# Performance work log

Measured on AMD Instinct MI355X. Metric: run time of the kernel, lower is better.

Reference implementation:

```python
import jax, jax.numpy as jnp
import numpy as np

N_NODES = 100000
N_EDGES = 3200000
IN_CH = 128
HID = 8
HEADS = 8
NEG_SLOPE = 0.2  # PyG GATConv default


def setup_inputs() -> dict:
    key = jax.random.key(0)
    ks = jax.random.split(key, 12)
    s = 0.1
    return {
        "x": jax.random.normal(ks[0], (N_NODES, IN_CH), jnp.float32),
        "edge_index": jax.random.randint(ks[1], (2, N_EDGES), 0, N_NODES, dtype=jnp.int64),
        "W1": jax.random.normal(ks[2], (IN_CH, HEADS * HID), jnp.float32) * s,
        "a_src1": jax.random.normal(ks[3], (1, HEADS, HID), jnp.float32) * s,
        "a_dst1": jax.random.normal(ks[4], (1, HEADS, HID), jnp.float32) * s,
        "b1": jax.random.normal(ks[5], (HEADS * HID,), jnp.float32) * s,
        "W2": jax.random.normal(ks[6], (HEADS * HID, HID), jnp.float32) * s,
        "a_src2": jax.random.normal(ks[7], (1, 1, HID), jnp.float32) * s,
        "a_dst2": jax.random.normal(ks[8], (1, 1, HID), jnp.float32) * s,
        "b2": jax.random.normal(ks[9], (HID,), jnp.float32) * s,
        "Wc": jax.random.normal(ks[10], (HID, 2), jnp.float32) * s,
        "bc": jax.random.normal(ks[11], (2,), jnp.float32) * s,
    }


def gat_conv(x, src, dst, W, a_src, a_dst, b, concat):
    """PyG-style GATConv (eval mode, self-loops already appended to src/dst)."""
    n = x.shape[0]
    H, C = a_src.shape[1], a_src.shape[2]
    h = (x @ W).reshape(n, H, C)                       # [N,H,C]
    alpha_src = jnp.sum(h * a_src, axis=-1)            # [N,H]
    alpha_dst = jnp.sum(h * a_dst, axis=-1)            # [N,H]
    e = jax.nn.leaky_relu(alpha_src[src] + alpha_dst[dst], NEG_SLOPE)  # [E,H]
    # segment softmax over destination-node neighborhoods
    m = jax.ops.segment_max(e, dst, num_segments=n)    # [N,H]
    m = jnp.where(jnp.isfinite(m), m, 0.0)
    p = jnp.exp(e - m[dst])
    z = jax.ops.segment_sum(p, dst, num_segments=n)    # [N,H]
    alpha = p / (z[dst] + 1e-16)                       # [E,H]
    out = jax.ops.segment_sum(alpha[..., None] * h[src], dst, num_segments=n)  # [N,H,C]
    out = out.reshape(n, H * C) if concat else out.mean(axis=1)
    return out + b


def reference(x, edge_index, W1, a_src1, a_dst1, b1, W2, a_src2, a_dst2, b2, Wc, bc):
    n = x.shape[0]
    loops = jnp.arange(n, dtype=edge_index.dtype)
    src = jnp.concatenate([edge_index[0], loops])
    dst = jnp.concatenate([edge_index[1], loops])
    h = jax.nn.relu(gat_conv(x, src, dst, W1, a_src1, a_dst1, b1, concat=True))
    embeddings = gat_conv(h, src, dst, W2, a_src2, a_dst2, b2, concat=False)
    logits = embeddings @ Wc + bc
    return embeddings, logits
```

## Files before the change

### kernel.cpp

```cpp
#include <hip/hip_runtime.h>
#include <hip/hip_bf16.h>
#include <hip/hip_fp16.h>

#define NN 100000
#define IN_CH 128
#define HID 8
#define HEADS 8
#define HC 64
#define BSH 8
#define NBUCK ((NN + 255) >> 8)
#define NBLK 512
#define PCAP 10240
#define LOG2E 1.44269504088896340736f

__device__ __forceinline__ unsigned short f2bf(float f) {
    unsigned u = __float_as_uint(f);
    unsigned r = (u + 0x7fffu + ((u >> 16) & 1u)) >> 16;
    return (unsigned short)r;
}


__global__ __launch_bounds__(256) void k_bincount(const int* __restrict__ ei, int E, int ET,
                                                  int cpb, int* __restrict__ cnt) {
    __shared__ int h[NBUCK];
    for (int i = threadIdx.x; i < NBUCK; i += 256) h[i] = 0;
    __syncthreads();
    int beg = blockIdx.x * cpb, end = min(ET, beg + cpb);
    for (int t = beg + threadIdx.x; t < end; t += 256) {
        int d = (t < E) ? ei[E + t] : (t - E);
        atomicAdd(&h[d >> BSH], 1);
    }
    __syncthreads();
    for (int i = threadIdx.x; i < NBUCK; i += 256) cnt[i * NBLK + blockIdx.x] = h[i];
}

__global__ __launch_bounds__(256) void k_colscan(int* __restrict__ cnt, int* __restrict__ btot) {
    __shared__ int sd[256];
    int t = threadIdx.x;
    int* col = cnt + blockIdx.x * NBLK;
    int v0 = col[2 * t], v1 = col[2 * t + 1];
    int s = v0 + v1;
    sd[t] = s;
    __syncthreads();
    for (int off = 1; off < 256; off <<= 1) {
        int u = (t >= off) ? sd[t - off] : 0;
        __syncthreads();
        sd[t] += u;
        __syncthreads();
    }
    int excl = sd[t] - s;
    col[2 * t] = excl;
    col[2 * t + 1] = excl + v0;
    if (t == 255) btot[blockIdx.x] = excl + s;
}

__global__ __launch_bounds__(256) void k_bucketbase(const int* __restrict__ btot,
                                                    int* __restrict__ bbase,
                                                    int* __restrict__ row_ptr) {
    __shared__ int sd[256];
    int t = threadIdx.x;
    int v0 = (2 * t < NBUCK) ? btot[2 * t] : 0;
    int v1 = (2 * t + 1 < NBUCK) ? btot[2 * t + 1] : 0;
    int s = v0 + v1;
    sd[t] = s;
    __syncthreads();
    for (int off = 1; off < 256; off <<= 1) {
        int u = (t >= off) ? sd[t - off] : 0;
        __syncthreads();
        sd[t] += u;
        __syncthreads();
    }
    int excl = sd[t] - s;
    if (2 * t < NBUCK) bbase[2 * t] = excl;
    if (2 * t + 1 < NBUCK) bbase[2 * t + 1] = excl + v0;
    if (t == 255) { bbase[NBUCK] = excl + s; row_ptr[NN] = excl + s; }
}

__global__ __launch_bounds__(256) void k_binscatter(const int* __restrict__ ei, int E, int ET,
                                                    int cpb, const int* __restrict__ cnt,
                                                    const int* __restrict__ bbase,
                                                    unsigned* __restrict__ pairs) {
    __shared__ int cur[NBUCK];
    for (int i = threadIdx.x; i < NBUCK; i += 256)
        cur[i] = bbase[i] + cnt[i * NBLK + blockIdx.x];
    __syncthreads();
    int beg = blockIdx.x * cpb, end = min(ET, beg + cpb);
    for (int t = beg + threadIdx.x; t < end; t += 256) {
        int s, d;
        if (t < E) { s = ei[t]; d = ei[E + t]; } else { s = t - E; d = t - E; }
        int pos = atomicAdd(&cur[d >> BSH], 1);
        pairs[pos] = ((unsigned)s << 8) | (unsigned)(d & 255);
    }
}

__global__ __launch_bounds__(256) void k_bucketscatter(const unsigned* __restrict__ pairs,
                                                       const int* __restrict__ bbase,
                                                       int* __restrict__ row_ptr,
                                                       int* __restrict__ csr) {
    __shared__ unsigned pl[PCAP];
    __shared__ int h[256];
    __shared__ int sd[256];
    int b = blockIdx.x;
    int t = threadIdx.x;
    int beg = bbase[b], end = bbase[b + 1];
    int cntE = end - beg;
    bool inl = cntE <= PCAP;
    if (inl)
        for (int j = t; j < cntE; j += 256) pl[j] = pairs[beg + j];
    h[t] = 0;
    __syncthreads();
    for (int j = t; j < cntE; j += 256) {
        unsigned pv = inl ? pl[j] : pairs[beg + j];
        atomicAdd(&h[pv & 255u], 1);
    }
    __syncthreads();
    int v = h[t];
    sd[t] = v;
    __syncthreads();
    for (int off = 1; off < 256; off <<= 1) {
        int u = (t >= off) ? sd[t - off] : 0;
        __syncthreads();
        sd[t] += u;
        __syncthreads();
    }
    int excl = sd[t] - v;
    int node = (b << 8) + t;
    if (node < NN) row_ptr[node] = beg + excl;
    __syncthreads();
    h[t] = beg + excl;
    __syncthreads();
    for (int j = t; j < cntE; j += 256) {
        unsigned pv = inl ? pl[j] : pairs[beg + j];
        int pos = atomicAdd(&h[pv & 255u], 1);
        csr[pos] = (int)(pv >> 8);
    }
}


__global__ __launch_bounds__(256) void k_gemm1(const float* __restrict__ x,
                                               const float* __restrict__ W1,
                                               const float* __restrict__ aS,
                                               const float* __restrict__ aD,
                                               unsigned* __restrict__ h1q,
                                               unsigned* __restrict__ asc1,
                                               float* __restrict__ adst1) {
    __shared__ float wl[IN_CH * HC];
    int tid = threadIdx.x;
    {
        const float4* Wg4 = (const float4*)W1;
        float4* wl4 = (float4*)wl;
#pragma unroll
        for (int i = 0; i < 8; ++i) wl4[tid + i * 256] = Wg4[tid + i * 256];
    }
    __syncthreads();
    int lane = tid & 63;
    int row = blockIdx.x * 16 + (tid >> 6) * 4 + (lane >> 4);
    int c0 = (lane & 15) * 4;
    const float4* xr = (const float4*)(x + (size_t)row * IN_CH);
    float4 acc = make_float4(0.f, 0.f, 0.f, 0.f);
#pragma unroll 4
    for (int kq = 0; kq < IN_CH / 4; ++kq) {
        float4 xv = xr[kq];
        const float4* wrow = (const float4*)(wl + (kq * 4) * HC + c0);
        float4 w0 = wrow[0];
        float4 w1 = wrow[HC / 4];
        float4 w2 = wrow[2 * (HC / 4)];
        float4 w3 = wrow[3 * (HC / 4)];
        acc.x += xv.x * w0.x + xv.y * w1.x + xv.z * w2.x + xv.w * w3.x;
        acc.y += xv.x * w0.y + xv.y * w1.y + xv.z * w2.y + xv.w * w3.y;
        acc.z += xv.x * w0.z + xv.y * w1.z + xv.z * w2.z + xv.w * w3.z;
        acc.w += xv.x * w0.w + xv.y * w1.w + xv.z * w2.w + xv.w * w3.w;
    }
    float am = fmaxf(fmaxf(fabsf(acc.x), fabsf(acc.y)), fmaxf(fabsf(acc.z), fabsf(acc.w)));
    am = fmaxf(am, __shfl_xor(am, 1, 64));
    am = fmaxf(am, __shfl_xor(am, 2, 64));
    am = fmaxf(am, __shfl_xor(am, 4, 64));
    am = fmaxf(am, __shfl_xor(am, 8, 64));
    am = fmaxf(am, 1e-20f);
    float qinv = 127.0f / am;
    int q0 = __float2int_rn(acc.x * qinv) + 128;
    int q1 = __float2int_rn(acc.y * qinv) + 128;
    int q2 = __float2int_rn(acc.z * qinv) + 128;
    int q3 = __float2int_rn(acc.w * qinv) + 128;
    unsigned u = (unsigned)q0 | ((unsigned)q1 << 8) | ((unsigned)q2 << 16) | ((unsigned)q3 << 24);
    h1q[row * 16 + (lane & 15)] = u;
    int head = (lane & 15) >> 1;
    int cl = c0 & 7;
    const float* as = aS + head * 8 + cl;
    const float* ad = aD + head * 8 + cl;
    float ps = acc.x * as[0] + acc.y * as[1] + acc.z * as[2] + acc.w * as[3];
    float pd = acc.x * ad[0] + acc.y * ad[1] + acc.z * ad[2] + acc.w * ad[3];
    ps += __shfl_xor(ps, 1, 64);
    pd += __shfl_xor(pd, 1, 64);
    if ((lane & 1) == 0) {
        unsigned lo = (unsigned)__half_as_ushort(__float2half(ps * LOG2E));
        unsigned hi = (unsigned)__half_as_ushort(__float2half(am * (1.0f / 127.0f)));
        asc1[row * 8 + head] = lo | (hi << 16);
        adst1[row * 8 + head] = pd * LOG2E;
    }
}


__global__ __launch_bounds__(256) void k_agg1(const int* __restrict__ row_ptr,
                                              const int* __restrict__ csr,
                                              const unsigned* __restrict__ asc1,
                                              const float* __restrict__ adst1,
                                              const uint2* __restrict__ h1q,
                                              const float* __restrict__ b1,
                                              const float* __restrict__ W2,
                                              const float* __restrict__ aS2,
                                              const float* __restrict__ aD2,
                                              unsigned short* __restrict__ h2bf,
                                              float* __restrict__ asrc2,
                                              float* __restrict__ adst2) {
    int tid = threadIdx.x;
    int lane = tid & 63;
    int slot = lane >> 3;
    int hl = lane & 7;
    float w2r[8];
#pragma unroll
    for (int i = 0; i < 8; ++i) w2r[i] = W2[(hl * 8 + i) * 8 + slot];
    float4 b0 = *(const float4*)(b1 + hl * 8);
    float4 b1v = *(const float4*)(b1 + hl * 8 + 4);
    float as2 = aS2[slot], ad2 = aD2[slot];
    int nbase = (blockIdx.x * 4 + (tid >> 6)) * 4;
    for (int ni = 0; ni < 4; ++ni) {
        int n = nbase + ni;
        float adst = adst1[n * 8 + hl];
        int beg = row_ptr[n], end = row_ptr[n + 1];
        int nit = (end - beg + 7) >> 3;
        float z = 0.f, zs = 0.f;
        float4 accA = make_float4(0.f, 0.f, 0.f, 0.f);
        float4 accB = make_float4(0.f, 0.f, 0.f, 0.f);
        int j0 = beg + slot;
        bool v0 = j0 < end;
        int s0 = v0 ? csr[j0] : 0;
        int j1 = j0 + 8;
        bool v1 = j1 < end;
        int s1 = v1 ? csr[j1] : 0;
        unsigned a0 = asc1[(size_t)s0 * 8 + hl];
        uint2 r0 = h1q[(size_t)s0 * 8 + hl];
        int jn = j1;
        for (int it = 0; it < nit; ++it) {
            int j2 = jn + 8;
            bool v2 = j2 < end;
            int s2 = v2 ? csr[j2] : 0;
            unsigned a1 = asc1[(size_t)s1 * 8 + hl];
            uint2 r1 = h1q[(size_t)s1 * 8 + hl];
            float e = __half2float(__ushort_as_half((unsigned short)(a0 & 0xffffu))) + adst;
            float csc = __half2float(__ushort_as_half((unsigned short)(a0 >> 16)));
            e = fmaxf(e, 0.2f * e);
            float p = v0 ? exp2f(e) : 0.f;
            float ps = p * csc;
            z += p;
            zs += ps;
            accA.x += ps * (float)(r0.x & 255u);
            accA.y += ps * (float)((r0.x >> 8) & 255u);
            accA.z += ps * (float)((r0.x >> 16) & 255u);
            accA.w += ps * (float)(r0.x >> 24);
            accB.x += ps * (float)(r0.y & 255u);
            accB.y += ps * (float)((r0.y >> 8) & 255u);
            accB.z += ps * (float)((r0.y >> 16) & 255u);
            accB.w += ps * (float)(r0.y >> 24);
            v0 = v1; a0 = a1; r0 = r1;
            v1 = v2; s1 = s2;
            jn = j2;
        }
#pragma unroll
        for (int off = 8; off <= 32; off <<= 1) {
            z += __shfl_xor(z, off, 64);
            zs += __shfl_xor(zs, off, 64);
            accA.x += __shfl_xor(accA.x, off, 64);
            accA.y += __shfl_xor(accA.y, off, 64);
            accA.z += __shfl_xor(accA.z, off, 64);
            accA.w += __shfl_xor(accA.w, off, 64);
            accB.x += __shfl_xor(accB.x, off, 64);
            accB.y += __shfl_xor(accB.y, off, 64);
            accB.z += __shfl_xor(accB.z, off, 64);
            accB.w += __shfl_xor(accB.w, off, 64);
        }
        float inv = 1.f / (z + 1e-16f);
        float zc = 128.f * zs;
        float hr0 = fmaxf((accA.x - zc) * inv + b0.x, 0.f);
        float hr1 = fmaxf((accA.y - zc) * inv + b0.y, 0.f);
        float hr2 = fmaxf((accA.z - zc) * inv + b0.z, 0.f);
        float hr3 = fmaxf((accA.w - zc) * inv + b0.w, 0.f);
        float hr4 = fmaxf((accB.x - zc) * inv + b1v.x, 0.f);
        float hr5 = fmaxf((accB.y - zc) * inv + b1v.y, 0.f);
        float hr6 = fmaxf((accB.z - zc) * inv + b1v.z, 0.f);
        float hr7 = fmaxf((accB.w - zc) * inv + b1v.w, 0.f);
        float part = hr0 * w2r[0] + hr1 * w2r[1] + hr2 * w2r[2] + hr3 * w2r[3] +
                     hr4 * w2r[4] + hr5 * w2r[5] + hr6 * w2r[6] + hr7 * w2r[7];
        part += __shfl_xor(part, 1, 64);
        part += __shfl_xor(part, 2, 64);
        part += __shfl_xor(part, 4, 64);
        if (hl == 0) {
            h2bf[(size_t)n * 8 + slot] = f2bf(part);
            float s2v = part * as2;
            float d2v = part * ad2;
            s2v += __shfl_xor(s2v, 8, 64);
            s2v += __shfl_xor(s2v, 16, 64);
            s2v += __shfl_xor(s2v, 32, 64);
            d2v += __shfl_xor(d2v, 8, 64);
            d2v += __shfl_xor(d2v, 16, 64);
            d2v += __shfl_xor(d2v, 32, 64);
            if (slot == 0) {
                asrc2[n] = s2v * LOG2E;
                adst2[n] = d2v * LOG2E;
            }
        }
    }
}


__global__ __launch_bounds__(256) void k_agg2(const int* __restrict__ row_ptr,
                                              const int* __restrict__ csr,
                                              const float* __restrict__ asrc2,
                                              const float* __restrict__ adst2,
                                              const unsigned short* __restrict__ h2bf,
                                              const float* __restrict__ b2,
                                              const float* __restrict__ Wc,
                                              const float* __restrict__ bc,
                                              float* __restrict__ out) {
    int tid = threadIdx.x;
    int lane = tid & 63;
    int n = blockIdx.x * 4 + (tid >> 6);
    int slot = lane >> 3;
    int sl = lane & 7;
    float adst = adst2[n];
    int beg = row_ptr[n], end = row_ptr[n + 1];
    int nit = (end - beg + 7) >> 3;
    float z = 0.f, acc = 0.f;
    int j0 = beg + slot;
    bool v0 = j0 < end;
    int s0 = v0 ? csr[j0] : 0;
    int j1 = j0 + 8;
    bool v1 = j1 < end;
    int s1 = v1 ? csr[j1] : 0;
    float a0 = asrc2[s0];
    unsigned short u0 = h2bf[(size_t)s0 * 8 + sl];
    int jn = j1;
    for (int it = 0; it < nit; ++it) {
        int j2 = jn + 8;
        bool v2 = j2 < end;
        int s2 = v2 ? csr[j2] : 0;
        float a1 = asrc2[s1];
        unsigned short u1 = h2bf[(size_t)s1 * 8 + sl];
        float e = a0 + adst;
        e = fmaxf(e, 0.2f * e);
        float p = v0 ? exp2f(e) : 0.f;
        float h0 = __uint_as_float(((unsigned)u0) << 16);
        z += p;
        acc += p * h0;
        v0 = v1; a0 = a1; u0 = u1;
        v1 = v2; s1 = s2;
        jn = j2;
    }
#pragma unroll
    for (int off = 8; off <= 32; off <<= 1) {
        z += __shfl_xor(z, off, 64);
        acc += __shfl_xor(acc, off, 64);
    }
    float emb = acc / (z + 1e-16f) + b2[sl];
    if (slot == 0) out[(size_t)n * HID + sl] = emb;
    float t0 = emb * Wc[sl * 2 + 0];
    float t1 = emb * Wc[sl * 2 + 1];
    t0 += __shfl_xor(t0, 1, 64); t0 += __shfl_xor(t0, 2, 64); t0 += __shfl_xor(t0, 4, 64);
    t1 += __shfl_xor(t1, 1, 64); t1 += __shfl_xor(t1, 2, 64); t1 += __shfl_xor(t1, 4, 64);
    if (lane == 0) {
        out[(size_t)NN * HID + n * 2 + 0] = t0 + bc[0];
        out[(size_t)NN * HID + n * 2 + 1] = t1 + bc[1];
    }
}


extern "C" void kernel_launch(void* const* d_in, const int* in_sizes, int n_in,
                              void* d_out, int out_size, void* d_ws, size_t ws_size,
                              hipStream_t stream) {
    const float* x  = (const float*)d_in[0];
    const int*   ei = (const int*)d_in[1];
    const float* W1 = (const float*)d_in[2];
    const float* aS = (const float*)d_in[3];
    const float* aD = (const float*)d_in[4];
    const float* b1 = (const float*)d_in[5];
    const float* W2 = (const float*)d_in[6];
    const float* aS2 = (const float*)d_in[7];
    const float* aD2 = (const float*)d_in[8];
    const float* b2 = (const float*)d_in[9];
    const float* Wc = (const float*)d_in[10];
    const float* bc = (const float*)d_in[11];

    int E = in_sizes[1] / 2;
    int N = NN;
    int ET = E + N;
    int cpb = (ET + NBLK - 1) / NBLK;

    char* p = (char*)d_ws;
    auto alloc = [&](size_t bytes) -> char* {
        char* r = p;
        p += (bytes + 255) & ~(size_t)255;
        return r;
    };
    unsigned* h1q   = (unsigned*)alloc((size_t)N * 16 * 4);
    unsigned* asc1  = (unsigned*)alloc((size_t)N * 8 * 4);
    float* adst1    = (float*)alloc((size_t)N * 8 * 4);
    unsigned short* h2bf = (unsigned short*)alloc((size_t)N * 8 * 2);
    float* asrc2    = (float*)alloc((size_t)N * 4);
    float* adst2    = (float*)alloc((size_t)N * 4);
    int*   row_ptr  = (int*)alloc((size_t)(N + 1) * 4);
    int*   cnt      = (int*)alloc((size_t)NBUCK * NBLK * 4);
    int*   btot     = (int*)alloc((size_t)NBUCK * 4);
    int*   bbase    = (int*)alloc((size_t)(NBUCK + 1) * 4);
    int*   csr      = (int*)alloc((size_t)ET * 4);
    unsigned* pairs = (unsigned*)alloc((size_t)ET * 4);

    k_bincount<<<NBLK, 256, 0, stream>>>(ei, E, ET, cpb, cnt);
    k_colscan<<<NBUCK, 256, 0, stream>>>(cnt, btot);
    k_bucketbase<<<1, 256, 0, stream>>>(btot, bbase, row_ptr);
    k_binscatter<<<NBLK, 256, 0, stream>>>(ei, E, ET, cpb, cnt, bbase, pairs);
    k_bucketscatter<<<NBUCK, 256, 0, stream>>>(pairs, bbase, row_ptr, csr);

    k_gemm1<<<N / 16, 256, 0, stream>>>(x, W1, aS, aD, h1q, asc1, adst1);
    k_agg1<<<N / 16, 256, 0, stream>>>(row_ptr, csr, asc1, adst1, (const uint2*)h1q,
                                       b1, W2, aS2, aD2, h2bf, asrc2, adst2);
    k_agg2<<<N / 4, 256, 0, stream>>>(row_ptr, csr, asrc2, adst2, h2bf, b2, Wc, bc,
                                      (float*)d_out);
}
```

Before: 240.4 us.

## Fuse CSR bucket scatter into layer-1 aggregation and split source score/scale arrays

Removes the separate bucket-scatter kernel and folds CSR construction into a new aggregation kernel. Each 256-node bucket is now handled by two blocks, one per 128-node half. Both blocks rebuild the bucket histogram and scan; each then scatters only its own half's edges into global CSR and, when they fit, into a shared-memory copy that its aggregation loop reads. The packed half-precision source score plus scale word becomes a separate fp16 array and a per-node float scale array. The goal is to drop a kernel launch and the global CSR re-read. In exchange there are far fewer, longer-running blocks with 32 nodes per wave processed serially, duplicated histogram work, and an extra per-edge gather for the scale.

```diff
diff --git a/kernel.cpp b/kernel.cpp
--- a/kernel.cpp
+++ b/kernel.cpp
@@ -10,7 +10,7 @@
 #define BSH 8
 #define NBUCK ((NN + 255) >> 8)
 #define NBLK 512
-#define PCAP 10240
+#define PCAP2 5120
 #define LOG2E 1.44269504088896340736f
 
 __device__ __forceinline__ unsigned short f2bf(float f) {
@@ -93,56 +93,14 @@
     }
 }
 
-__global__ __launch_bounds__(256) void k_bucketscatter(const unsigned* __restrict__ pairs,
-                                                       const int* __restrict__ bbase,
-                                                       int* __restrict__ row_ptr,
-                                                       int* __restrict__ csr) {
-    __shared__ unsigned pl[PCAP];
-    __shared__ int h[256];
-    __shared__ int sd[256];
-    int b = blockIdx.x;
-    int t = threadIdx.x;
-    int beg = bbase[b], end = bbase[b + 1];
-    int cntE = end - beg;
-    bool inl = cntE <= PCAP;
-    if (inl)
-        for (int j = t; j < cntE; j += 256) pl[j] = pairs[beg + j];
-    h[t] = 0;
-    __syncthreads();
-    for (int j = t; j < cntE; j += 256) {
-        unsigned pv = inl ? pl[j] : pairs[beg + j];
-        atomicAdd(&h[pv & 255u], 1);
-    }
-    __syncthreads();
-    int v = h[t];
-    sd[t] = v;
-    __syncthreads();
-    for (int off = 1; off < 256; off <<= 1) {
-        int u = (t >= off) ? sd[t - off] : 0;
-        __syncthreads();
-        sd[t] += u;
-        __syncthreads();
-    }
-    int excl = sd[t] - v;
-    int node = (b << 8) + t;
-    if (node < NN) row_ptr[node] = beg + excl;
-    __syncthreads();
-    h[t] = beg + excl;
-    __syncthreads();
-    for (int j = t; j < cntE; j += 256) {
-        unsigned pv = inl ? pl[j] : pairs[beg + j];
-        int pos = atomicAdd(&h[pv & 255u], 1);
-        csr[pos] = (int)(pv >> 8);
-    }
-}
-
 
 __global__ __launch_bounds__(256) void k_gemm1(const float* __restrict__ x,
                                                const float* __restrict__ W1,
                                                const float* __restrict__ aS,
                                                const float* __restrict__ aD,
                                                unsigned* __restrict__ h1q,
-                                               unsigned* __restrict__ asc1,
+                                               unsigned short* __restrict__ asrc1h,
+                                               float* __restrict__ scale1,
                                                float* __restrict__ adst1) {
     __shared__ float wl[IN_CH * HC];
     int tid = threadIdx.x;
@@ -193,28 +151,77 @@
     ps += __shfl_xor(ps, 1, 64);
     pd += __shfl_xor(pd, 1, 64);
     if ((lane & 1) == 0) {
-        unsigned lo = (unsigned)__half_as_ushort(__float2half(ps * LOG2E));
-        unsigned hi = (unsigned)__half_as_ushort(__float2half(am * (1.0f / 127.0f)));
-        asc1[row * 8 + head] = lo | (hi << 16);
+        asrc1h[row * 8 + head] = __half_as_ushort(__float2half(ps * LOG2E));
         adst1[row * 8 + head] = pd * LOG2E;
     }
-}
-
-
-__global__ __launch_bounds__(256) void k_agg1(const int* __restrict__ row_ptr,
-                                              const int* __restrict__ csr,
-                                              const unsigned* __restrict__ asc1,
-                                              const float* __restrict__ adst1,
-                                              const uint2* __restrict__ h1q,
-                                              const float* __restrict__ b1,
-                                              const float* __restrict__ W2,
-                                              const float* __restrict__ aS2,
-                                              const float* __restrict__ aD2,
-                                              unsigned short* __restrict__ h2bf,
-                                              float* __restrict__ asrc2,
-                                              float* __restrict__ adst2) {
-    int tid = threadIdx.x;
-    int lane = tid & 63;
+    if ((lane & 15) == 0) scale1[row] = am * (1.0f / 127.0f);
+}
+
+
+__global__ __launch_bounds__(256) void k_sortagg1(const unsigned* __restrict__ pairs,
+                                                  const int* __restrict__ bbase,
+                                                  int* __restrict__ row_ptr,
+                                                  int* __restrict__ csr,
+                                                  const unsigned short* __restrict__ asrc1h,
+                                                  const float* __restrict__ scale1,
+                                                  const float* __restrict__ adst1,
+                                                  const uint2* __restrict__ h1q,
+                                                  const float* __restrict__ b1,
+                                                  const float* __restrict__ W2,
+                                                  const float* __restrict__ aS2,
+                                                  const float* __restrict__ aD2,
+                                                  unsigned short* __restrict__ h2bf,
+                                                  float* __restrict__ asrc2,
+                                                  float* __restrict__ adst2) {
+    __shared__ int csr_l[PCAP2];
+    __shared__ int hist[256];
+    __shared__ int sdn[256];
+    __shared__ int rs[129];
+    int t = threadIdx.x;
+    int sb = blockIdx.x >> 1;
+    int hf = blockIdx.x & 1;
+    int beg = bbase[sb], end = bbase[sb + 1];
+    hist[t] = 0;
+    __syncthreads();
+    for (int j = beg + t; j < end; j += 256)
+        atomicAdd(&hist[pairs[j] & 255u], 1);
+    __syncthreads();
+    int v = hist[t];
+    sdn[t] = v;
+    __syncthreads();
+    for (int off = 1; off < 256; off <<= 1) {
+        int u = (t >= off) ? sdn[t - off] : 0;
+        __syncthreads();
+        sdn[t] += u;
+        __syncthreads();
+    }
+    int excl = sdn[t] - v;
+    int half0cnt = sdn[127];
+    int mybase = beg + (hf ? half0cnt : 0);
+    int myend = hf ? end : (beg + half0cnt);
+    bool inl = (myend - mybase) <= PCAP2;
+    bool own = (t >> 7) == hf;
+    if (own) {
+        int node = (sb << 8) + t;
+        if (node < NN) row_ptr[node] = beg + excl;
+        rs[t & 127] = beg + excl;
+        if ((t & 127) == 127) rs[128] = myend;
+    }
+    hist[t] = beg + excl;
+    __syncthreads();
+    for (int j = beg + t; j < end; j += 256) {
+        unsigned pv = pairs[j];
+        int d = (int)(pv & 255u);
+        if ((d >> 7) == hf) {
+            int pos = atomicAdd(&hist[d], 1);
+            int src = (int)(pv >> 8);
+            csr[pos] = src;
+            if (inl) csr_l[pos - mybase] = src;
+        }
+    }
+    __syncthreads();
+    int lane = t & 63;
+    int wv = t >> 6;
     int slot = lane >> 3;
     int hl = lane & 7;
     float w2r[8];
@@ -223,35 +230,34 @@
     float4 b0 = *(const float4*)(b1 + hl * 8);
     float4 b1v = *(const float4*)(b1 + hl * 8 + 4);
     float as2 = aS2[slot], ad2 = aD2[slot];
-    int nbase = (blockIdx.x * 4 + (tid >> 6)) * 4;
-    for (int ni = 0; ni < 4; ++ni) {
-        int n = nbase + ni;
-        float adst = adst1[n * 8 + hl];
-        int beg = row_ptr[n], end = row_ptr[n + 1];
-        int nit = (end - beg + 7) >> 3;
+    for (int i = 0; i < 32; ++i) {
+        int ln = wv * 32 + i;
+        int node = (sb << 8) + hf * 128 + ln;
+        if (node >= NN) break;
+        float adst = adst1[node * 8 + hl];
+        int jb = rs[ln] - mybase;
+        int je = rs[ln + 1] - mybase;
+        int nit = (je - jb + 7) >> 3;
         float z = 0.f, zs = 0.f;
         float4 accA = make_float4(0.f, 0.f, 0.f, 0.f);
         float4 accB = make_float4(0.f, 0.f, 0.f, 0.f);
-        int j0 = beg + slot;
-        bool v0 = j0 < end;
-        int s0 = v0 ? csr[j0] : 0;
-        int j1 = j0 + 8;
-        bool v1 = j1 < end;
-        int s1 = v1 ? csr[j1] : 0;
-        unsigned a0 = asc1[(size_t)s0 * 8 + hl];
+        int j = jb + slot;
+        bool v0 = j < je;
+        int s0 = v0 ? (inl ? csr_l[j] : csr[mybase + j]) : 0;
+        unsigned short a0 = asrc1h[(size_t)s0 * 8 + hl];
+        float c0s = scale1[s0];
         uint2 r0 = h1q[(size_t)s0 * 8 + hl];
-        int jn = j1;
         for (int it = 0; it < nit; ++it) {
-            int j2 = jn + 8;
-            bool v2 = j2 < end;
-            int s2 = v2 ? csr[j2] : 0;
-            unsigned a1 = asc1[(size_t)s1 * 8 + hl];
+            int j1 = j + 8;
+            bool v1 = j1 < je;
+            int s1 = v1 ? (inl ? csr_l[j1] : csr[mybase + j1]) : 0;
+            unsigned short a1 = asrc1h[(size_t)s1 * 8 + hl];
+            float c1s = scale1[s1];
             uint2 r1 = h1q[(size_t)s1 * 8 + hl];
-            float e = __half2float(__ushort_as_half((unsigned short)(a0 & 0xffffu))) + adst;
-            float csc = __half2float(__ushort_as_half((unsigned short)(a0 >> 16)));
+            float e = __half2float(__ushort_as_half(a0)) + adst;
             e = fmaxf(e, 0.2f * e);
             float p = v0 ? exp2f(e) : 0.f;
-            float ps = p * csc;
+            float ps = p * c0s;
             z += p;
             zs += ps;
             accA.x += ps * (float)(r0.x & 255u);
@@ -262,9 +268,8 @@
             accB.y += ps * (float)((r0.y >> 8) & 255u);
             accB.z += ps * (float)((r0.y >> 16) & 255u);
             accB.w += ps * (float)(r0.y >> 24);
-            v0 = v1; a0 = a1; r0 = r1;
-            v1 = v2; s1 = s2;
-            jn = j2;
+            v0 = v1; a0 = a1; c0s = c1s; r0 = r1;
+            j = j1;
         }
 #pragma unroll
         for (int off = 8; off <= 32; off <<= 1) {
@@ -295,7 +300,7 @@
         part += __shfl_xor(part, 2, 64);
         part += __shfl_xor(part, 4, 64);
         if (hl == 0) {
-            h2bf[(size_t)n * 8 + slot] = f2bf(part);
+            h2bf[(size_t)node * 8 + slot] = f2bf(part);
             float s2v = part * as2;
             float d2v = part * ad2;
             s2v += __shfl_xor(s2v, 8, 64);
@@ -305,8 +310,8 @@
             d2v += __shfl_xor(d2v, 16, 64);
             d2v += __shfl_xor(d2v, 32, 64);
             if (slot == 0) {
-                asrc2[n] = s2v * LOG2E;
-                adst2[n] = d2v * LOG2E;
+                asrc2[node] = s2v * LOG2E;
+                adst2[node] = d2v * LOG2E;
             }
         }
     }
@@ -402,7 +407,8 @@
         return r;
     };
     unsigned* h1q   = (unsigned*)alloc((size_t)N * 16 * 4);
-    unsigned* asc1  = (unsigned*)alloc((size_t)N * 8 * 4);
+    unsigned short* asrc1h = (unsigned short*)alloc((size_t)N * 8 * 2);
+    float* scale1   = (float*)alloc((size_t)N * 4);
     float* adst1    = (float*)alloc((size_t)N * 8 * 4);
     unsigned short* h2bf = (unsigned short*)alloc((size_t)N * 8 * 2);
     float* asrc2    = (float*)alloc((size_t)N * 4);
@@ -418,11 +424,11 @@
     k_colscan<<<NBUCK, 256, 0, stream>>>(cnt, btot);
     k_bucketbase<<<1, 256, 0, stream>>>(btot, bbase, row_ptr);
     k_binscatter<<<NBLK, 256, 0, stream>>>(ei, E, ET, cpb, cnt, bbase, pairs);
-    k_bucketscatter<<<NBUCK, 256, 0, stream>>>(pairs, bbase, row_ptr, csr);
-
-    k_gemm1<<<N / 16, 256, 0, stream>>>(x, W1, aS, aD, h1q, asc1, adst1);
-    k_agg1<<<N / 16, 256, 0, stream>>>(row_ptr, csr, asc1, adst1, (const uint2*)h1q,
-                                       b1, W2, aS2, aD2, h2bf, asrc2, adst2);
+
+    k_gemm1<<<N / 16, 256, 0, stream>>>(x, W1, aS, aD, h1q, asrc1h, scale1, adst1);
+    k_sortagg1<<<2 * NBUCK, 256, 0, stream>>>(pairs, bbase, row_ptr, csr,
+                                              asrc1h, scale1, adst1, (const uint2*)h1q,
+                                              b1, W2, aS2, aD2, h2bf, asrc2, adst2);
     k_agg2<<<N / 4, 256, 0, stream>>>(row_ptr, csr, asrc2, adst2, h2bf, b2, Wc, bc,
                                       (float*)d_out);
 }
```

Result: slower. 277.8 us (+15.6%).

## Register-block GEMM over four rows, split per-node scale, batch agg2 nodes

Applied to the files above, without the earlier changes.

k_gemm1 now computes four rows per thread, so each W1 value read from LDS is reused four times, and it launches 64 rows per block with a clamp for the tail. The per-head packed (alpha_src, scale) word is split into a half-precision alpha_src array plus one float scale per node, which shrinks the per-edge gather in k_agg1 but adds a second small scattered load per edge. k_agg2 processes four nodes per wavefront, cutting block count and hoisting the bias and classifier weight loads. The risks are higher register pressure in the GEMM and an extra memory transaction per edge in aggregation.

```diff
diff --git a/kernel.cpp b/kernel.cpp
--- a/kernel.cpp
+++ b/kernel.cpp
@@ -142,7 +142,8 @@
                                                const float* __restrict__ aS,
                                                const float* __restrict__ aD,
                                                unsigned* __restrict__ h1q,
-                                               unsigned* __restrict__ asc1,
+                                               unsigned short* __restrict__ asrc1h,
+                                               float* __restrict__ scale1,
                                                float* __restrict__ adst1) {
     __shared__ float wl[IN_CH * HC];
     int tid = threadIdx.x;
@@ -154,56 +155,86 @@
     }
     __syncthreads();
     int lane = tid & 63;
-    int row = blockIdx.x * 16 + (tid >> 6) * 4 + (lane >> 4);
+    int wv = tid >> 6;
+    int q = lane >> 4;
     int c0 = (lane & 15) * 4;
-    const float4* xr = (const float4*)(x + (size_t)row * IN_CH);
-    float4 acc = make_float4(0.f, 0.f, 0.f, 0.f);
-#pragma unroll 4
+    int base = blockIdx.x * 64 + wv * 16 + q * 4;
+    if (base + 4 > NN) base = NN - 4;
+    const float4* xr0 = (const float4*)(x + (size_t)(base + 0) * IN_CH);
+    const float4* xr1 = (const float4*)(x + (size_t)(base + 1) * IN_CH);
+    const float4* xr2 = (const float4*)(x + (size_t)(base + 2) * IN_CH);
+    const float4* xr3 = (const float4*)(x + (size_t)(base + 3) * IN_CH);
+    float4 ac0 = make_float4(0.f, 0.f, 0.f, 0.f);
+    float4 ac1 = ac0, ac2 = ac0, ac3 = ac0;
+#pragma unroll 2
     for (int kq = 0; kq < IN_CH / 4; ++kq) {
-        float4 xv = xr[kq];
         const float4* wrow = (const float4*)(wl + (kq * 4) * HC + c0);
         float4 w0 = wrow[0];
         float4 w1 = wrow[HC / 4];
         float4 w2 = wrow[2 * (HC / 4)];
         float4 w3 = wrow[3 * (HC / 4)];
-        acc.x += xv.x * w0.x + xv.y * w1.x + xv.z * w2.x + xv.w * w3.x;
-        acc.y += xv.x * w0.y + xv.y * w1.y + xv.z * w2.y + xv.w * w3.y;
-        acc.z += xv.x * w0.z + xv.y * w1.z + xv.z * w2.z + xv.w * w3.z;
-        acc.w += xv.x * w0.w + xv.y * w1.w + xv.z * w2.w + xv.w * w3.w;
-    }
-    float am = fmaxf(fmaxf(fabsf(acc.x), fabsf(acc.y)), fmaxf(fabsf(acc.z), fabsf(acc.w)));
-    am = fmaxf(am, __shfl_xor(am, 1, 64));
-    am = fmaxf(am, __shfl_xor(am, 2, 64));
-    am = fmaxf(am, __shfl_xor(am, 4, 64));
-    am = fmaxf(am, __shfl_xor(am, 8, 64));
-    am = fmaxf(am, 1e-20f);
-    float qinv = 127.0f / am;
-    int q0 = __float2int_rn(acc.x * qinv) + 128;
-    int q1 = __float2int_rn(acc.y * qinv) + 128;
-    int q2 = __float2int_rn(acc.z * qinv) + 128;
-    int q3 = __float2int_rn(acc.w * qinv) + 128;
-    unsigned u = (unsigned)q0 | ((unsigned)q1 << 8) | ((unsigned)q2 << 16) | ((unsigned)q3 << 24);
-    h1q[row * 16 + (lane & 15)] = u;
-    int head = (lane & 15) >> 1;
-    int cl = c0 & 7;
-    const float* as = aS + head * 8 + cl;
-    const float* ad = aD + head * 8 + cl;
-    float ps = acc.x * as[0] + acc.y * as[1] + acc.z * as[2] + acc.w * as[3];
-    float pd = acc.x * ad[0] + acc.y * ad[1] + acc.z * ad[2] + acc.w * ad[3];
-    ps += __shfl_xor(ps, 1, 64);
-    pd += __shfl_xor(pd, 1, 64);
-    if ((lane & 1) == 0) {
-        unsigned lo = (unsigned)__half_as_ushort(__float2half(ps * LOG2E));
-        unsigned hi = (unsigned)__half_as_ushort(__float2half(am * (1.0f / 127.0f)));
-        asc1[row * 8 + head] = lo | (hi << 16);
-        adst1[row * 8 + head] = pd * LOG2E;
+        float4 xv;
+        xv = xr0[kq];
+        ac0.x += xv.x * w0.x + xv.y * w1.x + xv.z * w2.x + xv.w * w3.x;
+        ac0.y += xv.x * w0.y + xv.y * w1.y + xv.z * w2.y + xv.w * w3.y;
+        ac0.z += xv.x * w0.z + xv.y * w1.z + xv.z * w2.z + xv.w * w3.z;
+        ac0.w += xv.x * w0.w + xv.y * w1.w + xv.z * w2.w + xv.w * w3.w;
+        xv = xr1[kq];
+        ac1.x += xv.x * w0.x + xv.y * w1.x + xv.z * w2.x + xv.w * w3.x;
+        ac1.y += xv.x * w0.y + xv.y * w1.y + xv.z * w2.y + xv.w * w3.y;
+        ac1.z += xv.x * w0.z + xv.y * w1.z + xv.z * w2.z + xv.w * w3.z;
+        ac1.w += xv.x * w0.w + xv.y * w1.w + xv.z * w2.w + xv.w * w3.w;
+        xv = xr2[kq];
+        ac2.x += xv.x * w0.x + xv.y * w1.x + xv.z * w2.x + xv.w * w3.x;
+        ac2.y += xv.x * w0.y + xv.y * w1.y + xv.z * w2.y + xv.w * w3.y;
+        ac2.z += xv.x * w0.z + xv.y * w1.z + xv.z * w2.z + xv.w * w3.z;
+        ac2.w += xv.x * w0.w + xv.y * w1.w + xv.z * w2.w + xv.w * w3.w;
+        xv = xr3[kq];
+        ac3.x += xv.x * w0.x + xv.y * w1.x + xv.z * w2.x + xv.w * w3.x;
+        ac3.y += xv.x * w0.y + xv.y * w1.y + xv.z * w2.y + xv.w * w3.y;
+        ac3.z += xv.x * w0.z + xv.y * w1.z + xv.z * w2.z + xv.w * w3.z;
+        ac3.w += xv.x * w0.w + xv.y * w1.w + xv.z * w2.w + xv.w * w3.w;
+    }
+    float4 accs[4] = {ac0, ac1, ac2, ac3};
+#pragma unroll
+    for (int r = 0; r < 4; ++r) {
+        float4 acc = accs[r];
+        int row = base + r;
+        float am = fmaxf(fmaxf(fabsf(acc.x), fabsf(acc.y)), fmaxf(fabsf(acc.z), fabsf(acc.w)));
+        am = fmaxf(am, __shfl_xor(am, 1, 64));
+        am = fmaxf(am, __shfl_xor(am, 2, 64));
+        am = fmaxf(am, __shfl_xor(am, 4, 64));
+        am = fmaxf(am, __shfl_xor(am, 8, 64));
+        am = fmaxf(am, 1e-20f);
+        float qinv = 127.0f / am;
+        int q0 = __float2int_rn(acc.x * qinv) + 128;
+        int q1 = __float2int_rn(acc.y * qinv) + 128;
+        int q2 = __float2int_rn(acc.z * qinv) + 128;
+        int q3 = __float2int_rn(acc.w * qinv) + 128;
+        unsigned u = (unsigned)q0 | ((unsigned)q1 << 8) | ((unsigned)q2 << 16) |
+                     ((unsigned)q3 << 24);
+        h1q[row * 16 + (lane & 15)] = u;
+        int head = (lane & 15) >> 1;
+        int cl = c0 & 7;
+        const float* as = aS + head * 8 + cl;
+        const float* ad = aD + head * 8 + cl;
+        float ps = acc.x * as[0] + acc.y * as[1] + acc.z * as[2] + acc.w * as[3];
+        float pd = acc.x * ad[0] + acc.y * ad[1] + acc.z * ad[2] + acc.w * ad[3];
+        ps += __shfl_xor(ps, 1, 64);
+        pd += __shfl_xor(pd, 1, 64);
+        if ((lane & 1) == 0) {
+            asrc1h[row * 8 + head] = __half_as_ushort(__float2half(ps * LOG2E));
+            adst1[row * 8 + head] = pd * LOG2E;
+        }
+        if ((lane & 15) == 0) scale1[row] = am * (1.0f / 127.0f);
     }
 }
 
 
 __global__ __launch_bounds__(256) void k_agg1(const int* __restrict__ row_ptr,
                                               const int* __restrict__ csr,
-                                              const unsigned* __restrict__ asc1,
+                                              const unsigned short* __restrict__ asrc1h,
+                                              const float* __restrict__ scale1,
                                               const float* __restrict__ adst1,
                                               const uint2* __restrict__ h1q,
                                               const float* __restrict__ b1,
@@ -238,20 +269,21 @@
         int j1 = j0 + 8;
         bool v1 = j1 < end;
         int s1 = v1 ? csr[j1] : 0;
-        unsigned a0 = asc1[(size_t)s0 * 8 + hl];
+        unsigned short a0 = asrc1h[(size_t)s0 * 8 + hl];
+        float c0s = scale1[s0];
         uint2 r0 = h1q[(size_t)s0 * 8 + hl];
         int jn = j1;
         for (int it = 0; it < nit; ++it) {
             int j2 = jn + 8;
             bool v2 = j2 < end;
             int s2 = v2 ? csr[j2] : 0;
-            unsigned a1 = asc1[(size_t)s1 * 8 + hl];
+            unsigned short a1 = asrc1h[(size_t)s1 * 8 + hl];
+            float c1s = scale1[s1];
             uint2 r1 = h1q[(size_t)s1 * 8 + hl];
-            float e = __half2float(__ushort_as_half((unsigned short)(a0 & 0xffffu))) + adst;
-            float csc = __half2float(__ushort_as_half((unsigned short)(a0 >> 16)));
+            float e = __half2float(__ushort_as_half(a0)) + adst;
             e = fmaxf(e, 0.2f * e);
             float p = v0 ? exp2f(e) : 0.f;
-            float ps = p * csc;
+            float ps = p * c0s;
             z += p;
             zs += ps;
             accA.x += ps * (float)(r0.x & 255u);
@@ -262,7 +294,7 @@
             accB.y += ps * (float)((r0.y >> 8) & 255u);
             accB.z += ps * (float)((r0.y >> 16) & 255u);
             accB.w += ps * (float)(r0.y >> 24);
-            v0 = v1; a0 = a1; r0 = r1;
+            v0 = v1; a0 = a1; c0s = c1s; r0 = r1;
             v1 = v2; s1 = s2;
             jn = j2;
         }
@@ -324,52 +356,57 @@
                                               float* __restrict__ out) {
     int tid = threadIdx.x;
     int lane = tid & 63;
-    int n = blockIdx.x * 4 + (tid >> 6);
     int slot = lane >> 3;
     int sl = lane & 7;
-    float adst = adst2[n];
-    int beg = row_ptr[n], end = row_ptr[n + 1];
-    int nit = (end - beg + 7) >> 3;
-    float z = 0.f, acc = 0.f;
-    int j0 = beg + slot;
-    bool v0 = j0 < end;
-    int s0 = v0 ? csr[j0] : 0;
-    int j1 = j0 + 8;
-    bool v1 = j1 < end;
-    int s1 = v1 ? csr[j1] : 0;
-    float a0 = asrc2[s0];
-    unsigned short u0 = h2bf[(size_t)s0 * 8 + sl];
-    int jn = j1;
-    for (int it = 0; it < nit; ++it) {
-        int j2 = jn + 8;
-        bool v2 = j2 < end;
-        int s2 = v2 ? csr[j2] : 0;
-        float a1 = asrc2[s1];
-        unsigned short u1 = h2bf[(size_t)s1 * 8 + sl];
-        float e = a0 + adst;
-        e = fmaxf(e, 0.2f * e);
-        float p = v0 ? exp2f(e) : 0.f;
-        float h0 = __uint_as_float(((unsigned)u0) << 16);
-        z += p;
-        acc += p * h0;
-        v0 = v1; a0 = a1; u0 = u1;
-        v1 = v2; s1 = s2;
-        jn = j2;
-    }
+    float b2v = b2[sl];
+    float wc0 = Wc[sl * 2 + 0], wc1 = Wc[sl * 2 + 1];
+    int nbase = (blockIdx.x * 4 + (tid >> 6)) * 4;
+    for (int ni = 0; ni < 4; ++ni) {
+        int n = nbase + ni;
+        float adst = adst2[n];
+        int beg = row_ptr[n], end = row_ptr[n + 1];
+        int nit = (end - beg + 7) >> 3;
+        float z = 0.f, acc = 0.f;
+        int j0 = beg + slot;
+        bool v0 = j0 < end;
+        int s0 = v0 ? csr[j0] : 0;
+        int j1 = j0 + 8;
+        bool v1 = j1 < end;
+        int s1 = v1 ? csr[j1] : 0;
+        float a0 = asrc2[s0];
+        unsigned short u0 = h2bf[(size_t)s0 * 8 + sl];
+        int jn = j1;
+        for (int it = 0; it < nit; ++it) {
+            int j2 = jn + 8;
+            bool v2 = j2 < end;
+            int s2 = v2 ? csr[j2] : 0;
+            float a1 = asrc2[s1];
+            unsigned short u1 = h2bf[(size_t)s1 * 8 + sl];
+            float e = a0 + adst;
+            e = fmaxf(e, 0.2f * e);
+            float p = v0 ? exp2f(e) : 0.f;
+            float h0 = __uint_as_float(((unsigned)u0) << 16);
+            z += p;
+            acc += p * h0;
+            v0 = v1; a0 = a1; u0 = u1;
+            v1 = v2; s1 = s2;
+            jn = j2;
+        }
 #pragma unroll
-    for (int off = 8; off <= 32; off <<= 1) {
-        z += __shfl_xor(z, off, 64);
-        acc += __shfl_xor(acc, off, 64);
-    }
-    float emb = acc / (z + 1e-16f) + b2[sl];
-    if (slot == 0) out[(size_t)n * HID + sl] = emb;
-    float t0 = emb * Wc[sl * 2 + 0];
-    float t1 = emb * Wc[sl * 2 + 1];
-    t0 += __shfl_xor(t0, 1, 64); t0 += __shfl_xor(t0, 2, 64); t0 += __shfl_xor(t0, 4, 64);
-    t1 += __shfl_xor(t1, 1, 64); t1 += __shfl_xor(t1, 2, 64); t1 += __shfl_xor(t1, 4, 64);
-    if (lane == 0) {
-        out[(size_t)NN * HID + n * 2 + 0] = t0 + bc[0];
-        out[(size_t)NN * HID + n * 2 + 1] = t1 + bc[1];
+        for (int off = 8; off <= 32; off <<= 1) {
+            z += __shfl_xor(z, off, 64);
+            acc += __shfl_xor(acc, off, 64);
+        }
+        float emb = acc / (z + 1e-16f) + b2v;
+        if (slot == 0) out[(size_t)n * HID + sl] = emb;
+        float t0 = emb * wc0;
+        float t1 = emb * wc1;
+        t0 += __shfl_xor(t0, 1, 64); t0 += __shfl_xor(t0, 2, 64); t0 += __shfl_xor(t0, 4, 64);
+        t1 += __shfl_xor(t1, 1, 64); t1 += __shfl_xor(t1, 2, 64); t1 += __shfl_xor(t1, 4, 64);
+        if (lane == 0) {
+            out[(size_t)NN * HID + n * 2 + 0] = t0 + bc[0];
+            out[(size_t)NN * HID + n * 2 + 1] = t1 + bc[1];
+        }
     }
 }
 
@@ -402,7 +439,8 @@
         return r;
     };
     unsigned* h1q   = (unsigned*)alloc((size_t)N * 16 * 4);
-    unsigned* asc1  = (unsigned*)alloc((size_t)N * 8 * 4);
+    unsigned short* asrc1h = (unsigned short*)alloc((size_t)N * 8 * 2);
+    float* scale1   = (float*)alloc((size_t)N * 4);
     float* adst1    = (float*)alloc((size_t)N * 8 * 4);
     unsigned short* h2bf = (unsigned short*)alloc((size_t)N * 8 * 2);
     float* asrc2    = (float*)alloc((size_t)N * 4);
@@ -420,9 +458,10 @@
     k_binscatter<<<NBLK, 256, 0, stream>>>(ei, E, ET, cpb, cnt, bbase, pairs);
     k_bucketscatter<<<NBUCK, 256, 0, stream>>>(pairs, bbase, row_ptr, csr);
 
-    k_gemm1<<<N / 16, 256, 0, stream>>>(x, W1, aS, aD, h1q, asc1, adst1);
-    k_agg1<<<N / 16, 256, 0, stream>>>(row_ptr, csr, asc1, adst1, (const uint2*)h1q,
-                                       b1, W2, aS2, aD2, h2bf, asrc2, adst2);
-    k_agg2<<<N / 4, 256, 0, stream>>>(row_ptr, csr, asrc2, adst2, h2bf, b2, Wc, bc,
-                                      (float*)d_out);
-}
+    k_gemm1<<<(N + 63) / 64, 256, 0, stream>>>(x, W1, aS, aD, h1q, asrc1h, scale1, adst1);
+    k_agg1<<<N / 16, 256, 0, stream>>>(row_ptr, csr, asrc1h, scale1, adst1,
+                                       (const uint2*)h1q, b1, W2, aS2, aD2,
+                                       h2bf, asrc2, adst2);
+    k_agg2<<<N / 16, 256, 0, stream>>>(row_ptr, csr, asrc2, adst2, h2bf, b2, Wc, bc,
+                                       (float*)d_out);
+}
```

New measurement: 227.3 us. -5.5%, faster.
